# Kernel optimization log

Measured on AMD Instinct MI355X. Metric: run time of the kernel, lower is better.

The kernel has to match this reference:

```python
import jax, jax.numpy as jnp
import numpy as np

C = 1.0          # Poincare ball curvature
NORM_FACTOR = 1.0
EPS = 1e-7
MAX_NORM = (1.0 - 1e-5) / np.sqrt(C)


def _artanh(x):
    x = jnp.clip(x, -1.0 + EPS, 1.0 - EPS)
    return jnp.arctanh(x)


def logmap0(x):
    # tangent vector at origin of Poincare ball (c=C)
    n = jnp.clip(jnp.linalg.norm(x, axis=-1, keepdims=True), EPS, None)
    sc = np.sqrt(C)
    return _artanh(sc * n) * x / (sc * n)


def expmap0(u):
    n = jnp.clip(jnp.linalg.norm(u, axis=-1, keepdims=True), EPS, None)
    sc = np.sqrt(C)
    return jnp.tanh(sc * n) * u / (sc * n)


def proj(x):
    # clip points to stay strictly inside the ball
    n = jnp.clip(jnp.linalg.norm(x, axis=-1, keepdims=True), EPS, None)
    return jnp.where(n > MAX_NORM, x / n * MAX_NORM, x)


def setup_inputs() -> dict:
    key = jax.random.key(0)
    ks = jax.random.split(key, 10)
    B, N, D_IN, D_H, D_LAT, L = 32, 1024, 128, 128, 64, 2
    s_in = 1.0 / np.sqrt(D_IN)
    s_h = 1.0 / np.sqrt(D_H)
    return {
        "node_features": jax.random.normal(ks[0], (B, N, D_IN), jnp.float32),
        "adjacency_matrix": jax.random.uniform(ks[1], (B, N, N), jnp.float32),
        "node_mask": jnp.ones((B, N, 1), jnp.float32),
        "W_embed": jax.random.normal(ks[2], (D_H, D_IN), jnp.float32) * s_in,
        "W_msg": jax.random.normal(ks[3], (L, D_H, D_H), jnp.float32) * s_h,
        "b_msg": jnp.zeros((L, D_H), jnp.float32),
        "W_agg": jax.random.normal(ks[4], (L, D_H, D_H), jnp.float32) * s_h,
        "b_agg": jnp.zeros((L, D_H), jnp.float32),
        "W_proj": jax.random.normal(ks[5], (2 * D_LAT, D_H), jnp.float32) * s_h,
        "b_proj": jnp.zeros((2 * D_LAT,), jnp.float32),
    }


def reference(node_features, adjacency_matrix, node_mask,
              W_embed, W_msg, b_msg, W_agg, b_agg, W_proj, b_proj):
    # feature embedding (bias-free linear, weights live on the manifold);
    # map to the Poincare ball
    h = jnp.einsum('bnd,hd->bnh', node_features, W_embed)
    x = proj(expmap0(h))

    num_layers = W_msg.shape[0]
    for l in range(num_layers):  # small fixed layer count
        t = logmap0(x)                                   # [B,N,D]
        m = t @ W_msg[l] + b_msg[l]                      # message transform
        agg = jnp.einsum('bij,bjd->bid', adjacency_matrix, m) / NORM_FACTOR
        agg = agg @ W_agg[l] + b_agg[l]                  # aggregation transform
        t = jax.nn.relu(m + agg)                         # tangent-space activation
        x = proj(expmap0(t))

    tangent = logmap0(x)                                 # final logmap0 in encode()
    mean_logvar = tangent @ W_proj.T + b_proj            # [B,N,2*latent]
    return mean_logvar * node_mask
```

## Files before the change

kernel.cpp:

```cpp
#include <hip/hip_runtime.h>
#include <hip/hip_bf16.h>

typedef __bf16 bf16;
typedef __bf16 bf16x8 __attribute__((ext_vector_type(8)));
typedef float  floatx4 __attribute__((ext_vector_type(4)));

#define EPSF    1e-7f
#define MAXNORM 0.99999f
#define TS_LD   136

__device__ __forceinline__ float hyp_scale(float ss) {
    float n  = sqrtf(ss);
    float nh = fmaxf(n, EPSF);
    float s1 = tanhf(nh) / nh;
    float nx = s1 * n;
    if (nx > MAXNORM) { s1 *= MAXNORM / nx; nx = MAXNORM; }
    float nx2 = fmaxf(nx, EPSF);
    return (atanhf(nx2) / nx2) * s1;
}

__device__ __forceinline__ bf16x8 cvt8(float4 a, float4 b) {
    bf16x8 r;
    r[0] = (bf16)a.x; r[1] = (bf16)a.y; r[2] = (bf16)a.z; r[3] = (bf16)a.w;
    r[4] = (bf16)b.x; r[5] = (bf16)b.y; r[6] = (bf16)b.z; r[7] = (bf16)b.w;
    return r;
}

__device__ __forceinline__ int sw128(int row, int k) {
    return row * 128 + (((k >> 3) ^ (row & 15)) << 3) + (k & 7);
}
__device__ __forceinline__ int sw64(int row, int k) {
    return row * 64 + (((k >> 3) ^ (row & 7)) << 3) + (k & 7);
}

__device__ __forceinline__ void gl_lds16(const void* g, void* l) {
    __builtin_amdgcn_global_load_lds(
        (__attribute__((address_space(1))) unsigned int*)(g),
        (__attribute__((address_space(3))) unsigned int*)(l), 16, 0, 0);
}

__global__ __launch_bounds__(256) void pack_adj(
    const float* __restrict__ Adj, bf16* __restrict__ AdjB)
{
    __shared__ __align__(16) bf16 Ls[4096 * 8];
    const int tid = threadIdx.x, bp = blockIdx.x;
    const int bmt = bp >> 2, q = bp & 3;
    const float* src = Adj + ((size_t)bmt << 17) + ((size_t)q << 15);

    #pragma unroll
    for (int i = 0; i < 16; ++i) {
        int gi = i * 256 + tid;
        int row = gi >> 7, gcol = gi & 127;
        int kk = gcol >> 3, gp = gcol & 7;
        const float4* p = reinterpret_cast<const float4*>(src + ((size_t)gi << 3));
        float4 v0 = p[0], v1 = p[1];
        int gpp = gp ^ (row & 7);
        *reinterpret_cast<bf16x8*>(&Ls[((kk * 32 + row) * 8 + gpp) * 8]) = cvt8(v0, v1);
    }
    __syncthreads();

    bf16* dst = AdjB + ((size_t)bmt << 17);
    #pragma unroll
    for (int i = 0; i < 16; ++i) {
        int go = i * 256 + tid;
        int kk = go >> 8, rem = go & 255;
        *reinterpret_cast<bf16x8*>(&dst[((((size_t)kk << 10) + (q << 8) + rem)) << 3]) =
            *reinterpret_cast<const bf16x8*>(&Ls[go * 8]);
    }
}

__global__ __launch_bounds__(256) void embed_msg(
    const float* __restrict__ X, const float* __restrict__ Wemb,
    const float* __restrict__ Wmsg, const float* __restrict__ bmsg,
    bf16* __restrict__ M, bf16* __restrict__ MT)
{
    __shared__ __align__(16) bf16 Xs[128 * 128];
    __shared__ __align__(16) bf16 Ws[128 * 128];
    __shared__ __align__(16) bf16 W2[128 * 128];
    __shared__ __align__(16) bf16 Ts[128 * TS_LD];
    const int tid = threadIdx.x, bx = blockIdx.x;

    {
        const float4* Xg = reinterpret_cast<const float4*>(X + (size_t)bx * 16384);
        #pragma unroll
        for (int i = 0; i < 8; ++i) {
            int g = tid + i * 256, row = g >> 4, gc = g & 15;
            float4 v0 = Xg[2 * g], v1 = Xg[2 * g + 1];
            *reinterpret_cast<bf16x8*>(&Xs[row * 128 + ((gc ^ (row & 15)) << 3)]) = cvt8(v0, v1);
        }
    }
    {
        const float4* Wg = reinterpret_cast<const float4*>(Wemb);
        #pragma unroll
        for (int i = 0; i < 8; ++i) {
            int g = tid + i * 256, row = g >> 4, gc = g & 15;
            float4 v0 = Wg[2 * g], v1 = Wg[2 * g + 1];
            *reinterpret_cast<bf16x8*>(&Ws[row * 128 + ((gc ^ (row & 15)) << 3)]) = cvt8(v0, v1);
        }
    }
    {
        const int c0 = (tid & 15) * 8;
        #pragma unroll
        for (int rr = 0; rr < 8; ++rr) {
            int r = (tid >> 4) * 8 + rr;
            const float4* p = reinterpret_cast<const float4*>(Wmsg + r * 128 + c0);
            float4 v0 = p[0], v1 = p[1];
            float vv[8] = {v0.x, v0.y, v0.z, v0.w, v1.x, v1.y, v1.z, v1.w};
            #pragma unroll
            for (int j = 0; j < 8; ++j) {
                int n = c0 + j;
                W2[n * 128 + (((r >> 3) ^ (n & 15)) << 3) + (r & 7)] = (bf16)vv[j];
            }
        }
    }
    __syncthreads();

    const int lane = tid & 63, wv = tid >> 6, n16 = lane & 15, quad = lane >> 4;
    const int rbase = wv * 32;

    floatx4 acc[2][8];
    #pragma unroll
    for (int a = 0; a < 2; ++a)
        #pragma unroll
        for (int c = 0; c < 8; ++c) acc[a][c] = (floatx4){0.f, 0.f, 0.f, 0.f};
    #pragma unroll
    for (int kc = 0; kc < 4; ++kc) {
        int k0 = kc * 32 + quad * 8;
        bf16x8 a0 = *reinterpret_cast<const bf16x8*>(&Xs[sw128(rbase + n16, k0)]);
        bf16x8 a1 = *reinterpret_cast<const bf16x8*>(&Xs[sw128(rbase + 16 + n16, k0)]);
        #pragma unroll
        for (int ct = 0; ct < 8; ++ct) {
            bf16x8 b = *reinterpret_cast<const bf16x8*>(&Ws[sw128(ct * 16 + n16, k0)]);
            acc[0][ct] = __builtin_amdgcn_mfma_f32_16x16x32_bf16(a0, b, acc[0][ct], 0, 0, 0);
            acc[1][ct] = __builtin_amdgcn_mfma_f32_16x16x32_bf16(a1, b, acc[1][ct], 0, 0, 0);
        }
    }
    #pragma unroll
    for (int rt = 0; rt < 2; ++rt) {
        #pragma unroll
        for (int r = 0; r < 4; ++r) {
            int row = rbase + rt * 16 + quad * 4 + r;
            float u[8], ss = 0.f;
            #pragma unroll
            for (int ct = 0; ct < 8; ++ct) { u[ct] = acc[rt][ct][r]; ss += u[ct] * u[ct]; }
            #pragma unroll
            for (int off = 1; off < 16; off <<= 1) ss += __shfl_xor(ss, off);
            float sc = hyp_scale(ss);
            #pragma unroll
            for (int ct = 0; ct < 8; ++ct)
                Ts[row * TS_LD + ct * 16 + n16] = (bf16)(u[ct] * sc);
        }
    }
    __syncthreads();

    floatx4 acc2[2][8];
    #pragma unroll
    for (int a = 0; a < 2; ++a)
        #pragma unroll
        for (int c = 0; c < 8; ++c) acc2[a][c] = (floatx4){0.f, 0.f, 0.f, 0.f};
    #pragma unroll
    for (int kc = 0; kc < 4; ++kc) {
        int k0 = kc * 32 + quad * 8;
        bf16x8 a0 = *reinterpret_cast<const bf16x8*>(&Ts[(rbase + n16) * TS_LD + k0]);
        bf16x8 a1 = *reinterpret_cast<const bf16x8*>(&Ts[(rbase + 16 + n16) * TS_LD + k0]);
        #pragma unroll
        for (int ct = 0; ct < 8; ++ct) {
            bf16x8 b = *reinterpret_cast<const bf16x8*>(&W2[sw128(ct * 16 + n16, k0)]);
            acc2[0][ct] = __builtin_amdgcn_mfma_f32_16x16x32_bf16(a0, b, acc2[0][ct], 0, 0, 0);
            acc2[1][ct] = __builtin_amdgcn_mfma_f32_16x16x32_bf16(a1, b, acc2[1][ct], 0, 0, 0);
        }
    }
    float bv[8];
    #pragma unroll
    for (int ct = 0; ct < 8; ++ct) bv[ct] = bmsg[ct * 16 + n16];
    #pragma unroll
    for (int rt = 0; rt < 2; ++rt) {
        #pragma unroll
        for (int r = 0; r < 4; ++r) {
            int lrow = rbase + rt * 16 + quad * 4 + r;
            size_t grow = (size_t)bx * 128 + lrow;
            #pragma unroll
            for (int ct = 0; ct < 8; ++ct) {
                bf16 o = (bf16)(acc2[rt][ct][r] + bv[ct]);
                M[grow * 128 + ct * 16 + n16] = o;
                MT[((grow >> 10) * 128 + ct * 16 + n16) * 1024 + (grow & 1023)] = o;
            }
        }
    }
}

template <int LAST>
__global__ __launch_bounds__(512) void adj_fast(
    const bf16* __restrict__ AdjB, const bf16* __restrict__ MT,
    const bf16* __restrict__ Mprev,
    const float* __restrict__ Wagg, const float* __restrict__ bagg,
    const float* __restrict__ W2f,  const float* __restrict__ b2,
    const float* __restrict__ Mask,
    bf16* __restrict__ Mout, bf16* __restrict__ MTout, float* __restrict__ Out)
{
    __shared__ __align__(16) bf16 smem[6 * 128 * 64];
    __shared__ __align__(16) bf16 Ts[128 * TS_LD];

    const int tid = threadIdx.x, bid = blockIdx.x;
    const int mt = bid >> 5, b = bid & 31;
    const bf16* Ab = AdjB + ((size_t)(b * 8 + mt) << 17);
    const bf16* Bg = MT + ((size_t)b << 17);

    const int lane = tid & 63, wv = tid >> 6, n16 = lane & 15, quad = lane >> 4;
    const int wr = (wv >> 2) * 64, wc = (wv & 3) * 32;

    bf16* As[3] = { smem,         smem + 8192,  smem + 16384 };
    bf16* Bs[3] = { smem + 24576, smem + 32768, smem + 40960 };

    floatx4 acc[4][2];
    #pragma unroll
    for (int a = 0; a < 4; ++a)
        #pragma unroll
        for (int c = 0; c < 2; ++c) acc[a][c] = (floatx4){0.f, 0.f, 0.f, 0.f};

    auto stage = [&](int kk, bf16* Adst, bf16* Bdst) {
        const bf16* at = Ab + (size_t)kk * 8192;
        #pragma unroll
        for (int j = 0; j < 2; ++j) {
            int base = wv * 128 + j * 64;
            gl_lds16(at + (size_t)(base + lane) * 8, Adst + base * 8);
            int gi = base + lane;
            int n = gi >> 3, gp = gi & 7;
            gl_lds16(Bg + (size_t)n * 1024 + kk * 64 + ((gp ^ (n & 7)) << 3),
                     Bdst + base * 8);
        }
    };

    stage(0, As[0], Bs[0]);
    stage(1, As[1], Bs[1]);
    #pragma unroll
    for (int p = 0; p < 16; ++p) {
        if (p < 15) asm volatile("s_waitcnt vmcnt(4)" ::: "memory");
        else        asm volatile("s_waitcnt vmcnt(0)" ::: "memory");
        __builtin_amdgcn_s_barrier();
        __builtin_amdgcn_sched_barrier(0);
        if (p + 2 < 16) stage(p + 2, As[(p + 2) % 3], Bs[(p + 2) % 3]);
        const bf16* Acur = As[p % 3];
        const bf16* Bcur = Bs[p % 3];
        #pragma unroll
        for (int kc = 0; kc < 2; ++kc) {
            int ko = kc * 32 + quad * 8;
            bf16x8 a[4], bb[2];
            #pragma unroll
            for (int rt = 0; rt < 4; ++rt)
                a[rt] = *reinterpret_cast<const bf16x8*>(&Acur[sw64(wr + rt * 16 + n16, ko)]);
            #pragma unroll
            for (int ct = 0; ct < 2; ++ct)
                bb[ct] = *reinterpret_cast<const bf16x8*>(&Bcur[sw64(wc + ct * 16 + n16, ko)]);
            __builtin_amdgcn_s_setprio(1);
            #pragma unroll
            for (int rt = 0; rt < 4; ++rt)
                #pragma unroll
                for (int ct = 0; ct < 2; ++ct)
                    acc[rt][ct] = __builtin_amdgcn_mfma_f32_16x16x32_bf16(a[rt], bb[ct], acc[rt][ct], 0, 0, 0);
            __builtin_amdgcn_s_setprio(0);
        }
    }
    __syncthreads();

    #pragma unroll
    for (int rt = 0; rt < 4; ++rt)
        #pragma unroll
        for (int ct = 0; ct < 2; ++ct)
            #pragma unroll
            for (int r = 0; r < 4; ++r) {
                int row = wr + rt * 16 + quad * 4 + r, col = wc + ct * 16 + n16;
                Ts[row * TS_LD + col] = (bf16)acc[rt][ct][r];
            }

    bf16* Wa = smem;
    bf16* W2 = smem + 128 * 128;
    {
        const int c0 = (tid & 15) * 8;
        #pragma unroll
        for (int rr = 0; rr < 4; ++rr) {
            int r = (tid >> 4) * 4 + rr;
            const float4* p = reinterpret_cast<const float4*>(Wagg + r * 128 + c0);
            float4 v0 = p[0], v1 = p[1];
            float vv[8] = {v0.x, v0.y, v0.z, v0.w, v1.x, v1.y, v1.z, v1.w};
            #pragma unroll
            for (int j = 0; j < 8; ++j) {
                int n = c0 + j;
                Wa[n * 128 + (((r >> 3) ^ (n & 15)) << 3) + (r & 7)] = (bf16)vv[j];
            }
        }
    }
    if (LAST) {
        const float4* Wg = reinterpret_cast<const float4*>(W2f);
        #pragma unroll
        for (int i = 0; i < 4; ++i) {
            int g = tid + i * 512, row = g >> 4, gc = g & 15;
            float4 v0 = Wg[2 * g], v1 = Wg[2 * g + 1];
            *reinterpret_cast<bf16x8*>(&W2[row * 128 + ((gc ^ (row & 15)) << 3)]) = cvt8(v0, v1);
        }
    } else {
        const int c0 = (tid & 15) * 8;
        #pragma unroll
        for (int rr = 0; rr < 4; ++rr) {
            int r = (tid >> 4) * 4 + rr;
            const float4* p = reinterpret_cast<const float4*>(W2f + r * 128 + c0);
            float4 v0 = p[0], v1 = p[1];
            float vv[8] = {v0.x, v0.y, v0.z, v0.w, v1.x, v1.y, v1.z, v1.w};
            #pragma unroll
            for (int j = 0; j < 8; ++j) {
                int n = c0 + j;
                W2[n * 128 + (((r >> 3) ^ (n & 15)) << 3) + (r & 7)] = (bf16)vv[j];
            }
        }
    }
    __syncthreads();

    const int rbase = wv * 16;
    const size_t growbase = (size_t)b * 1024 + (size_t)mt * 128;
    floatx4 acc2[8];
    #pragma unroll
    for (int c = 0; c < 8; ++c) acc2[c] = (floatx4){0.f, 0.f, 0.f, 0.f};
    #pragma unroll
    for (int kc = 0; kc < 4; ++kc) {
        int k0 = kc * 32 + quad * 8;
        bf16x8 a = *reinterpret_cast<const bf16x8*>(&Ts[(rbase + n16) * TS_LD + k0]);
        #pragma unroll
        for (int ct = 0; ct < 8; ++ct) {
            bf16x8 bb = *reinterpret_cast<const bf16x8*>(&Wa[sw128(ct * 16 + n16, k0)]);
            acc2[ct] = __builtin_amdgcn_mfma_f32_16x16x32_bf16(a, bb, acc2[ct], 0, 0, 0);
        }
    }
    {
        float bva[8];
        #pragma unroll
        for (int ct = 0; ct < 8; ++ct) bva[ct] = bagg[ct * 16 + n16];
        #pragma unroll
        for (int r = 0; r < 4; ++r) {
            int row = rbase + quad * 4 + r;
            size_t grow = growbase + row;
            float u[8], ss = 0.f;
            #pragma unroll
            for (int ct = 0; ct < 8; ++ct) {
                u[ct] = fmaxf(acc2[ct][r] + bva[ct] + (float)Mprev[grow * 128 + ct * 16 + n16], 0.f);
                ss += u[ct] * u[ct];
            }
            #pragma unroll
            for (int off = 1; off < 16; off <<= 1) ss += __shfl_xor(ss, off);
            float sc = hyp_scale(ss);
            #pragma unroll
            for (int ct = 0; ct < 8; ++ct)
                Ts[row * TS_LD + ct * 16 + n16] = (bf16)(u[ct] * sc);
        }
    }

    floatx4 acc3[8];
    #pragma unroll
    for (int c = 0; c < 8; ++c) acc3[c] = (floatx4){0.f, 0.f, 0.f, 0.f};
    #pragma unroll
    for (int kc = 0; kc < 4; ++kc) {
        int k0 = kc * 32 + quad * 8;
        bf16x8 a = *reinterpret_cast<const bf16x8*>(&Ts[(rbase + n16) * TS_LD + k0]);
        #pragma unroll
        for (int ct = 0; ct < 8; ++ct) {
            bf16x8 bb = *reinterpret_cast<const bf16x8*>(&W2[sw128(ct * 16 + n16, k0)]);
            acc3[ct] = __builtin_amdgcn_mfma_f32_16x16x32_bf16(a, bb, acc3[ct], 0, 0, 0);
        }
    }
    float bv2[8];
    #pragma unroll
    for (int ct = 0; ct < 8; ++ct) bv2[ct] = b2[ct * 16 + n16];
    #pragma unroll
    for (int r = 0; r < 4; ++r) {
        int row = rbase + quad * 4 + r;
        size_t grow = growbase + row;
        if (LAST) {
            float mk = Mask[grow];
            #pragma unroll
            for (int ct = 0; ct < 8; ++ct)
                Out[grow * 128 + ct * 16 + n16] = (acc3[ct][r] + bv2[ct]) * mk;
        } else {
            #pragma unroll
            for (int ct = 0; ct < 8; ++ct) {
                bf16 o = (bf16)(acc3[ct][r] + bv2[ct]);
                Mout[grow * 128 + ct * 16 + n16] = o;
                MTout[((grow >> 10) * 128 + ct * 16 + n16) * 1024 + (grow & 1023)] = o;
            }
        }
    }
}

template <int LAST>
__global__ __launch_bounds__(512) void adj_fused(
    const float* __restrict__ Adj, const bf16* __restrict__ MT,
    const bf16* __restrict__ Mprev,
    const float* __restrict__ Wagg, const float* __restrict__ bagg,
    const float* __restrict__ W2f,  const float* __restrict__ b2,
    const float* __restrict__ Mask,
    bf16* __restrict__ Mout, bf16* __restrict__ MTout, float* __restrict__ Out)
{
    __shared__ __align__(16) bf16 smem[4 * 128 * 64];
    __shared__ __align__(16) bf16 Ts[128 * TS_LD];
    bf16* As0 = smem;
    bf16* As1 = smem + 128 * 64;
    bf16* Bs0 = smem + 2 * 128 * 64;
    bf16* Bs1 = smem + 3 * 128 * 64;

    const int tid = threadIdx.x, bid = blockIdx.x;
    const int mt = bid >> 5, b = bid & 31;
    const float* Ag = Adj + ((size_t)b << 20) + ((size_t)mt << 17);
    const bf16*  Bg = MT  + ((size_t)b << 17);

    const int lane = tid & 63, wv = tid >> 6, n16 = lane & 15, quad = lane >> 4;
    const int wr = (wv >> 2) * 64, wc = (wv & 3) * 32;

    const int kk0 = (bid * 5 + (bid >> 5)) & 15;

    floatx4 acc[4][2];
    #pragma unroll
    for (int a = 0; a < 4; ++a)
        #pragma unroll
        for (int c = 0; c < 2; ++c) acc[a][c] = (floatx4){0.f, 0.f, 0.f, 0.f};

    float4 pa[2][2]; bf16x8 pb[2];
    auto load_regs = [&](int kk) {
        #pragma unroll
        for (int i = 0; i < 2; ++i) {
            int g = tid + i * 512, row = g >> 3, gc = g & 7;
            const float4* pA = reinterpret_cast<const float4*>(
                Ag + (size_t)row * 1024 + kk * 64 + gc * 8);
            pa[i][0] = pA[0]; pa[i][1] = pA[1];
            pb[i] = *reinterpret_cast<const bf16x8*>(Bg + (size_t)row * 1024 + kk * 64 + gc * 8);
        }
    };
    auto store_lds = [&](bf16* A, bf16* B) {
        #pragma unroll
        for (int i = 0; i < 2; ++i) {
            int g = tid + i * 512, row = g >> 3, gc = g & 7;
            *reinterpret_cast<bf16x8*>(&A[row * 64 + ((gc ^ (row & 7)) << 3)]) = cvt8(pa[i][0], pa[i][1]);
            *reinterpret_cast<bf16x8*>(&B[row * 64 + ((gc ^ (row & 7)) << 3)]) = pb[i];
        }
    };

    load_regs(kk0);
    store_lds(As0, Bs0);
    for (int p = 0; p < 16; ++p) {
        bf16* Acur = (p & 1) ? As1 : As0;
        bf16* Bcur = (p & 1) ? Bs1 : Bs0;
        bf16* Anxt = (p & 1) ? As0 : As1;
        bf16* Bnxt = (p & 1) ? Bs0 : Bs1;
        __syncthreads();
        if (p < 15) load_regs((p + 1 + kk0) & 15);
        #pragma unroll
        for (int kc = 0; kc < 2; ++kc) {
            int ko = kc * 32 + quad * 8;
            bf16x8 a[4], bb[2];
            #pragma unroll
            for (int rt = 0; rt < 4; ++rt)
                a[rt] = *reinterpret_cast<const bf16x8*>(&Acur[sw64(wr + rt * 16 + n16, ko)]);
            #pragma unroll
            for (int ct = 0; ct < 2; ++ct)
                bb[ct] = *reinterpret_cast<const bf16x8*>(&Bcur[sw64(wc + ct * 16 + n16, ko)]);
            #pragma unroll
            for (int rt = 0; rt < 4; ++rt)
                #pragma unroll
                for (int ct = 0; ct < 2; ++ct)
                    acc[rt][ct] = __builtin_amdgcn_mfma_f32_16x16x32_bf16(a[rt], bb[ct], acc[rt][ct], 0, 0, 0);
        }
        if (p < 15) store_lds(Anxt, Bnxt);
    }
    __syncthreads();

    #pragma unroll
    for (int rt = 0; rt < 4; ++rt)
        #pragma unroll
        for (int ct = 0; ct < 2; ++ct)
            #pragma unroll
            for (int r = 0; r < 4; ++r) {
                int row = wr + rt * 16 + quad * 4 + r, col = wc + ct * 16 + n16;
                Ts[row * TS_LD + col] = (bf16)acc[rt][ct][r];
            }

    bf16* Wa = smem;
    bf16* W2 = smem + 128 * 128;
    {
        const int c0 = (tid & 15) * 8;
        #pragma unroll
        for (int rr = 0; rr < 4; ++rr) {
            int r = (tid >> 4) * 4 + rr;
            const float4* p = reinterpret_cast<const float4*>(Wagg + r * 128 + c0);
            float4 v0 = p[0], v1 = p[1];
            float vv[8] = {v0.x, v0.y, v0.z, v0.w, v1.x, v1.y, v1.z, v1.w};
            #pragma unroll
            for (int j = 0; j < 8; ++j) {
                int n = c0 + j;
                Wa[n * 128 + (((r >> 3) ^ (n & 15)) << 3) + (r & 7)] = (bf16)vv[j];
            }
        }
    }
    if (LAST) {
        const float4* Wg = reinterpret_cast<const float4*>(W2f);
        #pragma unroll
        for (int i = 0; i < 4; ++i) {
            int g = tid + i * 512, row = g >> 4, gc = g & 15;
            float4 v0 = Wg[2 * g], v1 = Wg[2 * g + 1];
            *reinterpret_cast<bf16x8*>(&W2[row * 128 + ((gc ^ (row & 15)) << 3)]) = cvt8(v0, v1);
        }
    } else {
        const int c0 = (tid & 15) * 8;
        #pragma unroll
        for (int rr = 0; rr < 4; ++rr) {
            int r = (tid >> 4) * 4 + rr;
            const float4* p = reinterpret_cast<const float4*>(W2f + r * 128 + c0);
            float4 v0 = p[0], v1 = p[1];
            float vv[8] = {v0.x, v0.y, v0.z, v0.w, v1.x, v1.y, v1.z, v1.w};
            #pragma unroll
            for (int j = 0; j < 8; ++j) {
                int n = c0 + j;
                W2[n * 128 + (((r >> 3) ^ (n & 15)) << 3) + (r & 7)] = (bf16)vv[j];
            }
        }
    }
    __syncthreads();

    const int rbase = wv * 16;
    const size_t growbase = (size_t)b * 1024 + (size_t)mt * 128;
    floatx4 acc2[8];
    #pragma unroll
    for (int c = 0; c < 8; ++c) acc2[c] = (floatx4){0.f, 0.f, 0.f, 0.f};
    #pragma unroll
    for (int kc = 0; kc < 4; ++kc) {
        int k0 = kc * 32 + quad * 8;
        bf16x8 a = *reinterpret_cast<const bf16x8*>(&Ts[(rbase + n16) * TS_LD + k0]);
        #pragma unroll
        for (int ct = 0; ct < 8; ++ct) {
            bf16x8 bb = *reinterpret_cast<const bf16x8*>(&Wa[sw128(ct * 16 + n16, k0)]);
            acc2[ct] = __builtin_amdgcn_mfma_f32_16x16x32_bf16(a, bb, acc2[ct], 0, 0, 0);
        }
    }
    {
        float bva[8];
        #pragma unroll
        for (int ct = 0; ct < 8; ++ct) bva[ct] = bagg[ct * 16 + n16];
        #pragma unroll
        for (int r = 0; r < 4; ++r) {
            int row = rbase + quad * 4 + r;
            size_t grow = growbase + row;
            float u[8], ss = 0.f;
            #pragma unroll
            for (int ct = 0; ct < 8; ++ct) {
                u[ct] = fmaxf(acc2[ct][r] + bva[ct] + (float)Mprev[grow * 128 + ct * 16 + n16], 0.f);
                ss += u[ct] * u[ct];
            }
            #pragma unroll
            for (int off = 1; off < 16; off <<= 1) ss += __shfl_xor(ss, off);
            float sc = hyp_scale(ss);
            #pragma unroll
            for (int ct = 0; ct < 8; ++ct)
                Ts[row * TS_LD + ct * 16 + n16] = (bf16)(u[ct] * sc);
        }
    }

    floatx4 acc3[8];
    #pragma unroll
    for (int c = 0; c < 8; ++c) acc3[c] = (floatx4){0.f, 0.f, 0.f, 0.f};
    #pragma unroll
    for (int kc = 0; kc < 4; ++kc) {
        int k0 = kc * 32 + quad * 8;
        bf16x8 a = *reinterpret_cast<const bf16x8*>(&Ts[(rbase + n16) * TS_LD + k0]);
        #pragma unroll
        for (int ct = 0; ct < 8; ++ct) {
            bf16x8 bb = *reinterpret_cast<const bf16x8*>(&W2[sw128(ct * 16 + n16, k0)]);
            acc3[ct] = __builtin_amdgcn_mfma_f32_16x16x32_bf16(a, bb, acc3[ct], 0, 0, 0);
        }
    }
    float bv2[8];
    #pragma unroll
    for (int ct = 0; ct < 8; ++ct) bv2[ct] = b2[ct * 16 + n16];
    #pragma unroll
    for (int r = 0; r < 4; ++r) {
        int row = rbase + quad * 4 + r;
        size_t grow = growbase + row;
        if (LAST) {
            float mk = Mask[grow];
            #pragma unroll
            for (int ct = 0; ct < 8; ++ct)
                Out[grow * 128 + ct * 16 + n16] = (acc3[ct][r] + bv2[ct]) * mk;
        } else {
            #pragma unroll
            for (int ct = 0; ct < 8; ++ct) {
                bf16 o = (bf16)(acc3[ct][r] + bv2[ct]);
                Mout[grow * 128 + ct * 16 + n16] = o;
                MTout[((grow >> 10) * 128 + ct * 16 + n16) * 1024 + (grow & 1023)] = o;
            }
        }
    }
}

extern "C" void kernel_launch(void* const* d_in, const int* in_sizes, int n_in,
                              void* d_out, int out_size, void* d_ws, size_t ws_size,
                              hipStream_t stream)
{
    const float* X    = (const float*)d_in[0];
    const float* Adj  = (const float*)d_in[1];
    const float* Mask = (const float*)d_in[2];
    const float* Wemb = (const float*)d_in[3];
    const float* Wmsg = (const float*)d_in[4];
    const float* bmsg = (const float*)d_in[5];
    const float* Wagg = (const float*)d_in[6];
    const float* bagg = (const float*)d_in[7];
    const float* Wprj = (const float*)d_in[8];
    const float* bprj = (const float*)d_in[9];
    float* out = (float*)d_out;

    const size_t BN = 32768;
    bf16* m0   = (bf16*)d_ws;
    bf16* m0T  = m0  + BN * 128;
    bf16* m1   = m0T + BN * 128;
    bf16* m1T  = m1  + BN * 128;
    bf16* AdjB = m1T + BN * 128;

    const size_t need = (4 * BN * 128 + (size_t)33554432) * sizeof(bf16);

    if (ws_size >= need) {
        pack_adj<<<1024, 256, 0, stream>>>(Adj, AdjB);
        embed_msg<<<256, 256, 0, stream>>>(X, Wemb, Wmsg, bmsg, m0, m0T);
        adj_fast<0><<<256, 512, 0, stream>>>(AdjB, m0T, m0, Wagg, bagg,
                                             Wmsg + 16384, bmsg + 128, nullptr,
                                             m1, m1T, nullptr);
        adj_fast<1><<<256, 512, 0, stream>>>(AdjB, m1T, m1, Wagg + 16384, bagg + 128,
                                             Wprj, bprj, Mask,
                                             nullptr, nullptr, out);
    } else {
        embed_msg<<<256, 256, 0, stream>>>(X, Wemb, Wmsg, bmsg, m0, m0T);
        adj_fused<0><<<256, 512, 0, stream>>>(Adj, m0T, m0, Wagg, bagg,
                                              Wmsg + 16384, bmsg + 128, nullptr,
                                              m1, m1T, nullptr);
        adj_fused<1><<<256, 512, 0, stream>>>(Adj, m1T, m1, Wagg + 16384, bagg + 128,
                                              Wprj, bprj, Mask,
                                              nullptr, nullptr, out);
    }
}
```

Baseline: 317.8 us.

## Store transposed message matrix pre-swizzled via LDS for contiguous tile loads

The transposed message tensor MT is now written in a tiled, XOR-swizzled layout. Each tile is staged through shared memory and emitted as 16-byte vector stores, instead of scattered 2-byte strided writes. In the adjacency GEMM, this lets each B-tile stage be a contiguous global-to-LDS copy rather than strided row gathers. The old layout is kept in a legacy embed kernel for the fallback path that uses adj_fused. The cost is an extra barrier and LDS transpose pass in the producer epilogues.

```diff
diff --git a/kernel.cpp b/kernel.cpp
--- a/kernel.cpp
+++ b/kernel.cpp
@@ -38,6 +38,7 @@
         (__attribute__((address_space(1))) unsigned int*)(g),
         (__attribute__((address_space(3))) unsigned int*)(l), 16, 0, 0);
 }
+
 
 __global__ __launch_bounds__(256) void pack_adj(
     const float* __restrict__ Adj, bf16* __restrict__ AdjB)
@@ -181,10 +182,26 @@
             size_t grow = (size_t)bx * 128 + lrow;
             #pragma unroll
             for (int ct = 0; ct < 8; ++ct) {
+                int col = ct * 16 + n16;
                 bf16 o = (bf16)(acc2[rt][ct][r] + bv[ct]);
-                M[grow * 128 + ct * 16 + n16] = o;
-                MT[((grow >> 10) * 128 + ct * 16 + n16) * 1024 + (grow & 1023)] = o;
-            }
+                M[grow * 128 + col] = o;
+                Ts[lrow * TS_LD + col] = o;
+            }
+        }
+    }
+    __syncthreads();
+    {
+        const size_t mtb = (((size_t)(bx >> 3) * 16 + (size_t)(bx & 7) * 2) << 10);
+        #pragma unroll
+        for (int i = 0; i < 8; ++i) {
+            int g = i * 256 + tid;
+            int n = g & 127, rest = g >> 7, gp = rest & 7, kkl = rest >> 3;
+            int k0 = kkl * 64 + ((gp ^ (n & 7)) << 3);
+            bf16x8 v;
+            #pragma unroll
+            for (int j = 0; j < 8; ++j) v[j] = Ts[(k0 + j) * TS_LD + n];
+            size_t go = ((size_t)kkl << 10) + (n << 3) + gp;
+            *reinterpret_cast<bf16x8*>(MT + ((mtb + go) << 3)) = v;
         }
     }
 }
@@ -219,15 +236,13 @@
         for (int c = 0; c < 2; ++c) acc[a][c] = (floatx4){0.f, 0.f, 0.f, 0.f};
 
     auto stage = [&](int kk, bf16* Adst, bf16* Bdst) {
-        const bf16* at = Ab + (size_t)kk * 8192;
+        const bf16* at = Ab + ((size_t)kk << 13);
+        const bf16* bt = Bg + ((size_t)kk << 13);
         #pragma unroll
         for (int j = 0; j < 2; ++j) {
             int base = wv * 128 + j * 64;
             gl_lds16(at + (size_t)(base + lane) * 8, Adst + base * 8);
-            int gi = base + lane;
-            int n = gi >> 3, gp = gi & 7;
-            gl_lds16(Bg + (size_t)n * 1024 + kk * 64 + ((gp ^ (n & 7)) << 3),
-                     Bdst + base * 8);
+            gl_lds16(bt + (size_t)(base + lane) * 8, Bdst + base * 8);
         }
     };
 
@@ -381,9 +396,145 @@
         } else {
             #pragma unroll
             for (int ct = 0; ct < 8; ++ct) {
+                int col = ct * 16 + n16;
                 bf16 o = (bf16)(acc3[ct][r] + bv2[ct]);
-                Mout[grow * 128 + ct * 16 + n16] = o;
-                MTout[((grow >> 10) * 128 + ct * 16 + n16) * 1024 + (grow & 1023)] = o;
+                Mout[grow * 128 + col] = o;
+                Ts[row * TS_LD + col] = o;
+            }
+        }
+    }
+    if (!LAST) {
+        __syncthreads();
+        const size_t mtb = (((size_t)b * 16 + (size_t)mt * 2) << 10);
+        #pragma unroll
+        for (int i = 0; i < 4; ++i) {
+            int g = i * 512 + tid;
+            int n = g & 127, rest = g >> 7, gp = rest & 7, kkl = rest >> 3;
+            int k0 = kkl * 64 + ((gp ^ (n & 7)) << 3);
+            bf16x8 v;
+            #pragma unroll
+            for (int j = 0; j < 8; ++j) v[j] = Ts[(k0 + j) * TS_LD + n];
+            size_t go = ((size_t)kkl << 10) + (n << 3) + gp;
+            *reinterpret_cast<bf16x8*>(MTout + ((mtb + go) << 3)) = v;
+        }
+    }
+}
+
+__global__ __launch_bounds__(256) void embed_msg_legacy(
+    const float* __restrict__ X, const float* __restrict__ Wemb,
+    const float* __restrict__ Wmsg, const float* __restrict__ bmsg,
+    bf16* __restrict__ M, bf16* __restrict__ MT)
+{
+    __shared__ __align__(16) bf16 Xs[128 * 128];
+    __shared__ __align__(16) bf16 Ws[128 * 128];
+    __shared__ __align__(16) bf16 W2[128 * 128];
+    __shared__ __align__(16) bf16 Ts[128 * TS_LD];
+    const int tid = threadIdx.x, bx = blockIdx.x;
+
+    {
+        const float4* Xg = reinterpret_cast<const float4*>(X + (size_t)bx * 16384);
+        #pragma unroll
+        for (int i = 0; i < 8; ++i) {
+            int g = tid + i * 256, row = g >> 4, gc = g & 15;
+            float4 v0 = Xg[2 * g], v1 = Xg[2 * g + 1];
+            *reinterpret_cast<bf16x8*>(&Xs[row * 128 + ((gc ^ (row & 15)) << 3)]) = cvt8(v0, v1);
+        }
+    }
+    {
+        const float4* Wg = reinterpret_cast<const float4*>(Wemb);
+        #pragma unroll
+        for (int i = 0; i < 8; ++i) {
+            int g = tid + i * 256, row = g >> 4, gc = g & 15;
+            float4 v0 = Wg[2 * g], v1 = Wg[2 * g + 1];
+            *reinterpret_cast<bf16x8*>(&Ws[row * 128 + ((gc ^ (row & 15)) << 3)]) = cvt8(v0, v1);
+        }
+    }
+    {
+        const int c0 = (tid & 15) * 8;
+        #pragma unroll
+        for (int rr = 0; rr < 8; ++rr) {
+            int r = (tid >> 4) * 8 + rr;
+            const float4* p = reinterpret_cast<const float4*>(Wmsg + r * 128 + c0);
+            float4 v0 = p[0], v1 = p[1];
+            float vv[8] = {v0.x, v0.y, v0.z, v0.w, v1.x, v1.y, v1.z, v1.w};
+            #pragma unroll
+            for (int j = 0; j < 8; ++j) {
+                int n = c0 + j;
+                W2[n * 128 + (((r >> 3) ^ (n & 15)) << 3) + (r & 7)] = (bf16)vv[j];
+            }
+        }
+    }
+    __syncthreads();
+
+    const int lane = tid & 63, wv = tid >> 6, n16 = lane & 15, quad = lane >> 4;
+    const int rbase = wv * 32;
+
+    floatx4 acc[2][8];
+    #pragma unroll
+    for (int a = 0; a < 2; ++a)
+        #pragma unroll
+        for (int c = 0; c < 8; ++c) acc[a][c] = (floatx4){0.f, 0.f, 0.f, 0.f};
+    #pragma unroll
+    for (int kc = 0; kc < 4; ++kc) {
+        int k0 = kc * 32 + quad * 8;
+        bf16x8 a0 = *reinterpret_cast<const bf16x8*>(&Xs[sw128(rbase + n16, k0)]);
+        bf16x8 a1 = *reinterpret_cast<const bf16x8*>(&Xs[sw128(rbase + 16 + n16, k0)]);
+        #pragma unroll
+        for (int ct = 0; ct < 8; ++ct) {
+            bf16x8 b = *reinterpret_cast<const bf16x8*>(&Ws[sw128(ct * 16 + n16, k0)]);
+            acc[0][ct] = __builtin_amdgcn_mfma_f32_16x16x32_bf16(a0, b, acc[0][ct], 0, 0, 0);
+            acc[1][ct] = __builtin_amdgcn_mfma_f32_16x16x32_bf16(a1, b, acc[1][ct], 0, 0, 0);
+        }
+    }
+    #pragma unroll
+    for (int rt = 0; rt < 2; ++rt) {
+        #pragma unroll
+        for (int r = 0; r < 4; ++r) {
+            int row = rbase + rt * 16 + quad * 4 + r;
+            float u[8], ss = 0.f;
+            #pragma unroll
+            for (int ct = 0; ct < 8; ++ct) { u[ct] = acc[rt][ct][r]; ss += u[ct] * u[ct]; }
+            #pragma unroll
+            for (int off = 1; off < 16; off <<= 1) ss += __shfl_xor(ss, off);
+            float sc = hyp_scale(ss);
+            #pragma unroll
+            for (int ct = 0; ct < 8; ++ct)
+                Ts[row * TS_LD + ct * 16 + n16] = (bf16)(u[ct] * sc);
+        }
+    }
+    __syncthreads();
+
+    floatx4 acc2[2][8];
+    #pragma unroll
+    for (int a = 0; a < 2; ++a)
+        #pragma unroll
+        for (int c = 0; c < 8; ++c) acc2[a][c] = (floatx4){0.f, 0.f, 0.f, 0.f};
+    #pragma unroll
+    for (int kc = 0; kc < 4; ++kc) {
+        int k0 = kc * 32 + quad * 8;
+        bf16x8 a0 = *reinterpret_cast<const bf16x8*>(&Ts[(rbase + n16) * TS_LD + k0]);
+        bf16x8 a1 = *reinterpret_cast<const bf16x8*>(&Ts[(rbase + 16 + n16) * TS_LD + k0]);
+        #pragma unroll
+        for (int ct = 0; ct < 8; ++ct) {
+            bf16x8 b = *reinterpret_cast<const bf16x8*>(&W2[sw128(ct * 16 + n16, k0)]);
+            acc2[0][ct] = __builtin_amdgcn_mfma_f32_16x16x32_bf16(a0, b, acc2[0][ct], 0, 0, 0);
+            acc2[1][ct] = __builtin_amdgcn_mfma_f32_16x16x32_bf16(a1, b, acc2[1][ct], 0, 0, 0);
+        }
+    }
+    float bv[8];
+    #pragma unroll
+    for (int ct = 0; ct < 8; ++ct) bv[ct] = bmsg[ct * 16 + n16];
+    #pragma unroll
+    for (int rt = 0; rt < 2; ++rt) {
+        #pragma unroll
+        for (int r = 0; r < 4; ++r) {
+            int lrow = rbase + rt * 16 + quad * 4 + r;
+            size_t grow = (size_t)bx * 128 + lrow;
+            #pragma unroll
+            for (int ct = 0; ct < 8; ++ct) {
+                bf16 o = (bf16)(acc2[rt][ct][r] + bv[ct]);
+                M[grow * 128 + ct * 16 + n16] = o;
+                MT[((grow >> 10) * 128 + ct * 16 + n16) * 1024 + (grow & 1023)] = o;
             }
         }
     }
@@ -631,7 +782,7 @@
                                              Wprj, bprj, Mask,
                                              nullptr, nullptr, out);
     } else {
-        embed_msg<<<256, 256, 0, stream>>>(X, Wemb, Wmsg, bmsg, m0, m0T);
+        embed_msg_legacy<<<256, 256, 0, stream>>>(X, Wemb, Wmsg, bmsg, m0, m0T);
         adj_fused<0><<<256, 512, 0, stream>>>(Adj, m0T, m0, Wagg, bagg,
                                               Wmsg + 16384, bmsg + 128, nullptr,
                                               m1, m1T, nullptr);
```

New measurement: 335.4 us. 5.6% more time.
